# Optimization experiments

Measured on AMD Instinct MI355X. Metric: run time of the kernel, lower is better.

The kernel has to match this reference:

```python
import jax, jax.numpy as jnp
import numpy as np

HID = 1024
H = 8        # num_attention_heads
KV = 2       # num_key_value_heads
HD = HID // H  # head_dim = 128
G = H // KV    # kv groups = 4
EPS = 1e-6


def setup_inputs() -> dict:
    key = jax.random.key(0)
    ks = jax.random.split(key, 12)
    B, S = 4, 2048
    s = 0.02
    inp = {
        "hidden_states": jax.random.normal(ks[0], (B, S, HID), jnp.float32),
        "rope": jax.random.normal(ks[1], (1, 1, S, 2 * HD), jnp.float32),
        # q_proj outputs 2*H*HD (query + elementwise gate)
        "Wq": jax.random.normal(ks[2], (HID, 2 * H * HD), jnp.float32) * s,
        "bq": jnp.zeros((2 * H * HD,), jnp.float32),
        "Wk": jax.random.normal(ks[3], (HID, KV * HD), jnp.float32) * s,
        "bk": jnp.zeros((KV * HD,), jnp.float32),
        "Wv": jax.random.normal(ks[4], (HID, KV * HD), jnp.float32) * s,
        "bv": jnp.zeros((KV * HD,), jnp.float32),
        "Wo": jax.random.normal(ks[5], (H * HD, HID), jnp.float32) * s,
        "bo": jnp.zeros((HID,), jnp.float32),
        "q_norm_w": jnp.ones((HD,), jnp.float32),
        "k_norm_w": jnp.ones((HD,), jnp.float32),
    }
    return inp


def _rmsnorm(x, w):
    var = jnp.mean(jnp.square(x), axis=-1, keepdims=True)
    return x * jax.lax.rsqrt(var + EPS) * w


def _rot(x):
    # interleaved rotation: [-x1, x0, -x3, x2, ...]
    x2 = x.reshape(x.shape[:-1] + (HD // 2, 2))
    r = jnp.stack([-x2[..., 1], x2[..., 0]], axis=-1)
    return r.reshape(x.shape)


def _apply_rope_cat(x, emb):
    # emb: [S, 2*HD] = cat(sin, cos); x: [B, h, S, HD]
    sin, cos = jnp.split(emb, 2, axis=-1)
    sin = sin[None, None]
    cos = cos[None, None]
    return x * cos + _rot(x) * sin


def reference(hidden_states, rope, Wq, bq, Wk, bk, Wv, bv, Wo, bo, q_norm_w, k_norm_w):
    B, S, _ = hidden_states.shape
    qg = hidden_states @ Wq + bq                     # [B,S,2*H*HD]
    qg = qg.reshape(B, S, KV, -1)                    # [B,S,KV, 2*G*HD]
    q, gate = jnp.split(qg, [HD * G], axis=-1)       # [B,S,KV,G*HD], [B,S,KV,G*HD]
    gate = gate.reshape(B, S, H, HD)                 # [B,S,H,HD]
    q = q.reshape(B, S, H, HD).transpose(0, 2, 1, 3) # [B,H,S,HD]
    k = (hidden_states @ Wk + bk).reshape(B, S, KV, HD).transpose(0, 2, 1, 3)
    v = (hidden_states @ Wv + bv).reshape(B, S, KV, HD).transpose(0, 2, 1, 3)

    q = _rmsnorm(q, q_norm_w)
    k = _rmsnorm(k, k_norm_w)

    emb = rope[0, 0, :S]                             # [S, 2*HD]
    q = _apply_rope_cat(q, emb)
    k = _apply_rope_cat(k, emb)

    # GQA: repeat kv heads to match query heads
    k = jnp.repeat(k, G, axis=1)                     # [B,H,S,HD]
    v = jnp.repeat(v, G, axis=1)

    scale = 1.0 / jnp.sqrt(jnp.asarray(HD, q.dtype))
    scores = jnp.einsum("bhqd,bhkd->bhqk", q, k) * scale
    attn = jax.nn.softmax(scores, axis=-1)
    out = jnp.einsum("bhqk,bhkd->bhqd", attn, v)     # [B,H,S,HD]

    out = out.transpose(0, 2, 1, 3)                  # [B,S,H,HD]
    out = out * jax.nn.sigmoid(gate)
    out = out.reshape(B, S, H * HD)
    return out @ Wo + bo
```

## Files before the change

kernel.cpp:

```cpp
#include <hip/hip_runtime.h>
#include <math.h>

#define SCALE_ 0.08838834764831845f
#define PSHIFT 8.0f

typedef __attribute__((ext_vector_type(8))) short short8;
typedef __attribute__((ext_vector_type(4))) float floatx4;
typedef __attribute__((ext_vector_type(4))) _Float16 half4;
typedef __attribute__((ext_vector_type(8))) _Float16 half8;

__device__ inline short f2bf(float x) {
    union { float f; unsigned u; } v; v.f = x;
    unsigned r = v.u + 0x7fff + ((v.u >> 16) & 1);
    return (short)(r >> 16);
}
__device__ inline float bf2f(short h) {
    union { float f; unsigned u; } v; v.u = ((unsigned)(unsigned short)h) << 16;
    return v.f;
}

__global__ __launch_bounds__(256) void convert_x(
    const float* __restrict__ X, short* __restrict__ Xb,
    const float* __restrict__ bq, const float* __restrict__ bk2,
    const float* __restrict__ bv2, float* __restrict__ bcat)
{
    const int gid = blockIdx.x * 256 + threadIdx.x;
    if (gid < 2097152) {
        const float4 v = ((const float4*)X)[gid];
        short4 o;
        o.x = f2bf(v.x); o.y = f2bf(v.y); o.z = f2bf(v.z); o.w = f2bf(v.w);
        ((short4*)Xb)[gid] = o;
    }
    if (gid < 2560)
        bcat[gid] = (gid < 2048) ? bq[gid]
                  : (gid < 2304) ? bk2[gid - 2048] : bv2[gid - 2304];
}

__global__ __launch_bounds__(256) void wtrans(
    const float* __restrict__ Wq, const float* __restrict__ Wk,
    const float* __restrict__ Wv, const float* __restrict__ Wo,
    short* __restrict__ Wt, short* __restrict__ Wot)
{
    __shared__ float T[32][33];
    const int t = threadIdx.x;
    const int k0 = blockIdx.x * 32;
    const int ny = blockIdx.y;
    const float* src; int ldn, ncol0, nrow0; short* dst;
    if (ny < 80) {
        const int n0 = ny * 32;
        if (n0 < 2048)      { src = Wq; ldn = 2048; ncol0 = n0; }
        else if (n0 < 2304) { src = Wk; ldn = 256;  ncol0 = n0 - 2048; }
        else                { src = Wv; ldn = 256;  ncol0 = n0 - 2304; }
        dst = Wt; nrow0 = n0;
    } else {
        const int n0 = (ny - 80) * 32;
        src = Wo; ldn = 1024; ncol0 = n0; dst = Wot; nrow0 = n0;
    }
    {
        const int r = t >> 3, c4 = (t & 7) * 4;
        const float4 v = *(const float4*)&src[(size_t)(k0 + r) * ldn + ncol0 + c4];
        T[r][c4 + 0] = v.x; T[r][c4 + 1] = v.y; T[r][c4 + 2] = v.z; T[r][c4 + 3] = v.w;
    }
    __syncthreads();
    {
        const int nr = t >> 3, kc4 = (t & 7) * 4;
        short4 o;
        o.x = f2bf(T[kc4 + 0][nr]);
        o.y = f2bf(T[kc4 + 1][nr]);
        o.z = f2bf(T[kc4 + 2][nr]);
        o.w = f2bf(T[kc4 + 3][nr]);
        *(short4*)&dst[(size_t)(nrow0 + nr) * 1024 + k0 + kc4] = o;
    }
}

__global__ __launch_bounds__(256) void qkv_mfma(
    const short* __restrict__ Ag, const short* __restrict__ Bg,
    const float* __restrict__ bcat,
    short* __restrict__ qb, short* __restrict__ kb,
    short* __restrict__ vb, short* __restrict__ gateb)
{
    __shared__ short As[128 * 64];
    __shared__ short Bs[128 * 64];
    const int tid = threadIdx.x;
    const int wave = tid >> 6, lane = tid & 63;
    const int quad = lane >> 4, l16 = lane & 15;
    const int wm = wave & 1, wn = wave >> 1;
    const int m0 = blockIdx.y * 128, n0 = blockIdx.x * 128;

    floatx4 acc[4][4] = {};

    for (int k0 = 0; k0 < 1024; k0 += 64) {
        __syncthreads();
        #pragma unroll
        for (int c = 0; c < 4; ++c) {
            const int blk = (c * 4 + wave) * 64 + lane;
            const int row = blk >> 3, p = blk & 7;
            const int col = (p ^ (row & 7)) << 3;
            __builtin_amdgcn_global_load_lds(
                (const __attribute__((address_space(1))) unsigned int*)(Ag + (size_t)(m0 + row) * 1024 + k0 + col),
                (__attribute__((address_space(3))) unsigned int*)&As[(c * 4 + wave) * 512],
                16, 0, 0);
            __builtin_amdgcn_global_load_lds(
                (const __attribute__((address_space(1))) unsigned int*)(Bg + (size_t)(n0 + row) * 1024 + k0 + col),
                (__attribute__((address_space(3))) unsigned int*)&Bs[(c * 4 + wave) * 512],
                16, 0, 0);
        }
        __syncthreads();
        #pragma unroll
        for (int ks = 0; ks < 2; ++ks) {
            short8 af[4], bfr[4];
            #pragma unroll
            for (int mt = 0; mt < 4; ++mt) {
                const int row = wm * 64 + mt * 16 + l16;
                const int p = (ks * 4 + quad) ^ (row & 7);
                af[mt] = *(const short8*)&As[row * 64 + p * 8];
            }
            #pragma unroll
            for (int nt = 0; nt < 4; ++nt) {
                const int row = wn * 64 + nt * 16 + l16;
                const int p = (ks * 4 + quad) ^ (row & 7);
                bfr[nt] = *(const short8*)&Bs[row * 64 + p * 8];
            }
            #pragma unroll
            for (int mt = 0; mt < 4; ++mt)
                #pragma unroll
                for (int nt = 0; nt < 4; ++nt)
                    acc[mt][nt] = __builtin_amdgcn_mfma_f32_16x16x32_bf16(af[mt], bfr[nt], acc[mt][nt], 0, 0, 0);
        }
    }

    #pragma unroll
    for (int nt = 0; nt < 4; ++nt) {
        const int n = n0 + wn * 64 + nt * 16 + l16;
        const float bias = bcat[n];
        #pragma unroll
        for (int mt = 0; mt < 4; ++mt) {
            #pragma unroll
            for (int r = 0; r < 4; ++r) {
                const int m = m0 + wm * 64 + mt * 16 + quad * 4 + r;
                const int b = m >> 11, s = m & 2047;
                const short o = f2bf(acc[mt][nt][r] + bias);
                if (n < 2048) {
                    const int kv = n >> 10, rr = n & 1023;
                    if (rr < 512) {
                        const int h = kv * 4 + (rr >> 7), d = rr & 127;
                        qb[(((size_t)(b * 8 + h)) * 2048 + s) * 128 + d] = o;
                    } else {
                        const int r2 = rr - 512;
                        const int h = kv * 4 + (r2 >> 7), d = r2 & 127;
                        gateb[(size_t)m * 1024 + h * 128 + d] = o;
                    }
                } else if (n < 2304) {
                    const int c = n - 2048;
                    kb[(((size_t)(b * 2 + (c >> 7))) * 2048 + s) * 128 + (c & 127)] = o;
                } else {
                    const int c = n - 2304;
                    vb[(((size_t)(b * 2 + (c >> 7))) * 2048 + s) * 128 + (c & 127)] = o;
                }
            }
        }
    }
}

__global__ __launch_bounds__(256) void norm_rope(
    short* __restrict__ qb, short* __restrict__ kb,
    const float* __restrict__ rope,
    const float* __restrict__ qw, const float* __restrict__ kw)
{
    const int row = blockIdx.x * 4 + (threadIdx.x >> 6);
    short* base; const float* w; int s; float scl;
    if (row < 65536) { base = qb + (size_t)row * 128; s = row & 2047; w = qw; scl = SCALE_; }
    else { const int r2 = row - 65536; base = kb + (size_t)r2 * 128; s = r2 & 2047; w = kw; scl = 1.0f; }
    const int lane = threadIdx.x & 63;
    const short2 xv = *(const short2*)&base[lane * 2];
    const float x0 = bf2f(xv.x), x1 = bf2f(xv.y);
    float ssq = x0 * x0 + x1 * x1;
    #pragma unroll
    for (int off = 1; off < 64; off <<= 1) ssq += __shfl_xor(ssq, off);
    const float inv = rsqrtf(ssq * (1.0f / 128.0f) + 1e-6f);
    const float a = x0 * inv * w[lane * 2];
    const float b = x1 * inv * w[lane * 2 + 1];
    const float* er = rope + (size_t)s * 256;
    const float sin0 = er[lane * 2], sin1 = er[lane * 2 + 1];
    const float cos0 = er[128 + lane * 2], cos1 = er[128 + lane * 2 + 1];
    short2 o;
    o.x = f2bf((a * cos0 - b * sin0) * scl);
    o.y = f2bf((b * cos1 + a * sin1) * scl);
    *(short2*)&base[lane * 2] = o;
}

__global__ __launch_bounds__(256) void vtrans(
    const short* __restrict__ vb, _Float16* __restrict__ vt)
{
    __shared__ float T[32][33];
    const int t = threadIdx.x;
    const int s0 = blockIdx.x * 32, d0 = blockIdx.y * 32, bk = blockIdx.z;
    const short* src = vb + ((size_t)bk * 2048 + s0) * 128 + d0;
    {
        const int sr = t >> 3, c4 = (t & 7) * 4;
        const short4 xv = *(const short4*)&src[sr * 128 + c4];
        T[sr][c4 + 0] = bf2f(xv.x);
        T[sr][c4 + 1] = bf2f(xv.y);
        T[sr][c4 + 2] = bf2f(xv.z);
        T[sr][c4 + 3] = bf2f(xv.w);
    }
    __syncthreads();
    {
        const int dr = t >> 3, sc4 = (t & 7) * 4;
        const int cs = sc4 >> 2;
        const int nc = (cs < 4) ? (cs << 1) : (((cs - 4) << 1) | 1);
        half4 o;
        o[0] = (_Float16)T[sc4 + 0][dr];
        o[1] = (_Float16)T[sc4 + 1][dr];
        o[2] = (_Float16)T[sc4 + 2][dr];
        o[3] = (_Float16)T[sc4 + 3][dr];
        *(half4*)&vt[((size_t)bk * 128 + d0 + dr) * 2048 + s0 + nc * 4] = o;
    }
}

__global__ __launch_bounds__(256, 2) void attn_mfma(
    const short* __restrict__ qb, const short* __restrict__ kb,
    const _Float16* __restrict__ vt, const short* __restrict__ gateb,
    short* __restrict__ xo)
{
    __shared__ short    Ks[2][64 * 128];
    __shared__ _Float16 VTs[2][128 * 64];

    const int tid = threadIdx.x;
    const int wave = tid >> 6, lane = tid & 63;
    const int quad = lane >> 4, l16 = lane & 15;
    const int bh = blockIdx.y, b = bh >> 3, h = bh & 7, kv = h >> 2;
    const int q0 = blockIdx.x * 128;

    short8 qf[4][2];
    #pragma unroll
    for (int u = 0; u < 2; ++u) {
        const short* qbase = qb + (((size_t)(b * 8 + h)) * 2048 + q0 + wave * 32 + u * 16 + l16) * 128;
        #pragma unroll
        for (int ks = 0; ks < 4; ++ks)
            qf[ks][u] = *(const short8*)&qbase[ks * 32 + quad * 8];
    }

    const short*    kbase  = kb + (size_t)(b * 2 + kv) * 2048 * 128;
    const _Float16* vtbase = vt + (size_t)(b * 2 + kv) * 128 * 2048;

    int koff[4], voff[4];
    #pragma unroll
    for (int c = 0; c < 4; ++c) {
        const int idx = (c * 4 + wave) * 64 + lane;
        { const int r = idx >> 4, p = idx & 15;
          koff[c] = r * 128 + ((p ^ (r & 7)) << 3); }
        { const int r = idx >> 3, p = idx & 7;
          voff[c] = r * 2048 + ((p ^ (r & 7)) << 3); }
    }

    floatx4 O[8][2] = {};
    float lsum[2] = {0.0f, 0.0f};

    #pragma unroll
    for (int c = 0; c < 4; ++c) {
        __builtin_amdgcn_global_load_lds(
            (const __attribute__((address_space(1))) unsigned int*)(kbase + koff[c]),
            (__attribute__((address_space(3))) unsigned int*)&Ks[0][(c * 4 + wave) * 512],
            16, 0, 0);
        __builtin_amdgcn_global_load_lds(
            (const __attribute__((address_space(1))) unsigned int*)(vtbase + voff[c]),
            (__attribute__((address_space(3))) unsigned int*)&VTs[0][(c * 4 + wave) * 512],
            16, 0, 0);
    }

    for (int kt = 0; kt < 32; ++kt) {
        const int cur = kt & 1;
        __syncthreads();

        if (kt + 1 < 32) {
            const short*    kg = kbase  + (size_t)(kt + 1) * 8192;
            const _Float16* vg = vtbase + (kt + 1) * 64;
            #pragma unroll
            for (int c = 0; c < 4; ++c) {
                __builtin_amdgcn_global_load_lds(
                    (const __attribute__((address_space(1))) unsigned int*)(kg + koff[c]),
                    (__attribute__((address_space(3))) unsigned int*)&Ks[cur ^ 1][(c * 4 + wave) * 512],
                    16, 0, 0);
                __builtin_amdgcn_global_load_lds(
                    (const __attribute__((address_space(1))) unsigned int*)(vg + voff[c]),
                    (__attribute__((address_space(3))) unsigned int*)&VTs[cur ^ 1][(c * 4 + wave) * 512],
                    16, 0, 0);
            }
        }

        #pragma unroll
        for (int t = 0; t < 2; ++t) {
            floatx4 ST[2][2];
            #pragma unroll
            for (int j = 0; j < 2; ++j) {
                ST[j][0] = (floatx4){0.f, 0.f, 0.f, 0.f};
                ST[j][1] = (floatx4){0.f, 0.f, 0.f, 0.f};
                const int krow = (2 * t + j) * 16 + l16;
                #pragma unroll
                for (int ks = 0; ks < 4; ++ks) {
                    const short8 af = *(const short8*)&Ks[cur][krow * 128 + (((ks * 4 + quad) ^ (l16 & 7)) << 3)];
                    ST[j][0] = __builtin_amdgcn_mfma_f32_16x16x32_bf16(af, qf[ks][0], ST[j][0], 0, 0, 0);
                    ST[j][1] = __builtin_amdgcn_mfma_f32_16x16x32_bf16(af, qf[ks][1], ST[j][1], 0, 0, 0);
                }
            }

            half8 pf[2];
            #pragma unroll
            for (int u = 0; u < 2; ++u) {
                #pragma unroll
                for (int r = 0; r < 4; ++r) {
                    const float plo = __expf(ST[0][u][r] - PSHIFT);
                    const float phi = __expf(ST[1][u][r] - PSHIFT);
                    lsum[u] += plo + phi;
                    pf[u][r]     = (_Float16)plo;
                    pf[u][4 + r] = (_Float16)phi;
                }
            }

            #pragma unroll
            for (int dt = 0; dt < 8; ++dt) {
                const half8 va = *(const half8*)&VTs[cur][(dt * 16 + l16) * 64 + (((4 * t + quad) ^ (l16 & 7)) << 3)];
                O[dt][0] = __builtin_amdgcn_mfma_f32_16x16x32_f16(va, pf[0], O[dt][0], 0, 0, 0);
                O[dt][1] = __builtin_amdgcn_mfma_f32_16x16x32_f16(va, pf[1], O[dt][1], 0, 0, 0);
            }
        }
    }

    #pragma unroll
    for (int u = 0; u < 2; ++u) {
        float ps = lsum[u];
        ps += __shfl_xor(ps, 16);
        ps += __shfl_xor(ps, 32);
        const float invl = 1.0f / ps;
        const int s = q0 + wave * 32 + u * 16 + l16;
        const size_t base = ((size_t)b * 2048 + s) * 1024 + h * 128;
        #pragma unroll
        for (int dt = 0; dt < 8; ++dt) {
            const int d0 = dt * 16 + quad * 4;
            const short4 g4 = *(const short4*)&gateb[base + d0];
            short4 o4;
            o4.x = f2bf(O[dt][u][0] * invl * (1.0f / (1.0f + __expf(-bf2f(g4.x)))));
            o4.y = f2bf(O[dt][u][1] * invl * (1.0f / (1.0f + __expf(-bf2f(g4.y)))));
            o4.z = f2bf(O[dt][u][2] * invl * (1.0f / (1.0f + __expf(-bf2f(g4.z)))));
            o4.w = f2bf(O[dt][u][3] * invl * (1.0f / (1.0f + __expf(-bf2f(g4.w)))));
            *(short4*)&xo[base + d0] = o4;
        }
    }
}

__global__ __launch_bounds__(256) void out_mfma(
    const short* __restrict__ Ag, const short* __restrict__ Bg,
    const float* __restrict__ bo, float* __restrict__ Y)
{
    __shared__ short As[128 * 64];
    __shared__ short Bs[128 * 64];
    const int tid = threadIdx.x;
    const int wave = tid >> 6, lane = tid & 63;
    const int quad = lane >> 4, l16 = lane & 15;
    const int wm = wave & 1, wn = wave >> 1;
    const int m0 = blockIdx.y * 128, n0 = blockIdx.x * 128;

    floatx4 acc[4][4] = {};

    for (int k0 = 0; k0 < 1024; k0 += 64) {
        __syncthreads();
        #pragma unroll
        for (int c = 0; c < 4; ++c) {
            const int blk = (c * 4 + wave) * 64 + lane;
            const int row = blk >> 3, p = blk & 7;
            const int col = (p ^ (row & 7)) << 3;
            __builtin_amdgcn_global_load_lds(
                (const __attribute__((address_space(1))) unsigned int*)(Ag + (size_t)(m0 + row) * 1024 + k0 + col),
                (__attribute__((address_space(3))) unsigned int*)&As[(c * 4 + wave) * 512],
                16, 0, 0);
            __builtin_amdgcn_global_load_lds(
                (const __attribute__((address_space(1))) unsigned int*)(Bg + (size_t)(n0 + row) * 1024 + k0 + col),
                (__attribute__((address_space(3))) unsigned int*)&Bs[(c * 4 + wave) * 512],
                16, 0, 0);
        }
        __syncthreads();
        #pragma unroll
        for (int ks = 0; ks < 2; ++ks) {
            short8 af[4], bfr[4];
            #pragma unroll
            for (int mt = 0; mt < 4; ++mt) {
                const int row = wm * 64 + mt * 16 + l16;
                const int p = (ks * 4 + quad) ^ (row & 7);
                af[mt] = *(const short8*)&As[row * 64 + p * 8];
            }
            #pragma unroll
            for (int nt = 0; nt < 4; ++nt) {
                const int row = wn * 64 + nt * 16 + l16;
                const int p = (ks * 4 + quad) ^ (row & 7);
                bfr[nt] = *(const short8*)&Bs[row * 64 + p * 8];
            }
            #pragma unroll
            for (int mt = 0; mt < 4; ++mt)
                #pragma unroll
                for (int nt = 0; nt < 4; ++nt)
                    acc[mt][nt] = __builtin_amdgcn_mfma_f32_16x16x32_bf16(af[mt], bfr[nt], acc[mt][nt], 0, 0, 0);
        }
    }

    #pragma unroll
    for (int nt = 0; nt < 4; ++nt) {
        const int n = n0 + wn * 64 + nt * 16 + l16;
        const float bias = bo[n];
        #pragma unroll
        for (int mt = 0; mt < 4; ++mt) {
            #pragma unroll
            for (int r = 0; r < 4; ++r) {
                const int m = m0 + wm * 64 + mt * 16 + quad * 4 + r;
                Y[(size_t)m * 1024 + n] = acc[mt][nt][r] + bias;
            }
        }
    }
}

extern "C" void kernel_launch(void* const* d_in, const int* in_sizes, int n_in,
                              void* d_out, int out_size, void* d_ws, size_t ws_size,
                              hipStream_t stream) {
    (void)in_sizes; (void)n_in; (void)out_size; (void)ws_size;
    const float* hs   = (const float*)d_in[0];
    const float* rope = (const float*)d_in[1];
    const float* Wq   = (const float*)d_in[2];
    const float* bq   = (const float*)d_in[3];
    const float* Wk   = (const float*)d_in[4];
    const float* bk   = (const float*)d_in[5];
    const float* Wv   = (const float*)d_in[6];
    const float* bv   = (const float*)d_in[7];
    const float* Wo   = (const float*)d_in[8];
    const float* bo   = (const float*)d_in[9];
    const float* qw   = (const float*)d_in[10];
    const float* kw   = (const float*)d_in[11];
    float* out = (float*)d_out;

    short* qb    = (short*)d_ws;
    short* kbuf  = qb    + (size_t)8388608;
    short* vb    = kbuf  + (size_t)2097152;
    _Float16* vt = (_Float16*)(vb + (size_t)2097152);
    short* gateb = (short*)(vt + (size_t)2097152);
    short* xb    = gateb + (size_t)8388608;
    short* wt    = xb    + (size_t)8388608;
    short* wot   = wt    + (size_t)2621440;
    float* bcat  = (float*)(wot + (size_t)1048576);

    convert_x<<<dim3(8192), 256, 0, stream>>>(hs, xb, bq, bk, bv, bcat);
    wtrans<<<dim3(32, 112), 256, 0, stream>>>(Wq, Wk, Wv, Wo, wt, wot);
    qkv_mfma<<<dim3(20, 64), 256, 0, stream>>>(xb, wt, bcat, qb, kbuf, vb, gateb);
    norm_rope<<<dim3(20480), 256, 0, stream>>>(qb, kbuf, rope, qw, kw);
    vtrans<<<dim3(64, 4, 8), 256, 0, stream>>>(vb, vt);
    attn_mfma<<<dim3(16, 32), 256, 0, stream>>>(qb, kbuf, vt, gateb, xb);
    out_mfma<<<dim3(8, 64), 256, 0, stream>>>(xb, wot, bo, out);
}
```

Before: 298.3 us.

## Merge prep kernels, remap blocks for XCD locality, add MFMA priority and exp2 softmax

Combines convert_x with wtrans, and norm_rope with vtrans, so two launches are saved. The GEMM and attention grids are linearised and remapped so that blocks sharing A rows or a head land on the same XCD, which should improve L2 reuse. The attention inner loop raises wave priority around its MFMA sections and computes exp with exp2f of an FMA. These changes mix launch-overhead, locality and scheduling ideas, and the remaps depend on the eight-XCD round-robin dispatch assumption.

```diff
diff --git a/kernel.cpp b/kernel.cpp
--- a/kernel.cpp
+++ b/kernel.cpp
@@ -3,6 +3,8 @@
 
 #define SCALE_ 0.08838834764831845f
 #define PSHIFT 8.0f
+#define LOG2E_ 1.4426950408889634f
+#define PSH2_  11.541560327111707f
 
 typedef __attribute__((ext_vector_type(8))) short short8;
 typedef __attribute__((ext_vector_type(4))) float floatx4;
@@ -19,32 +21,33 @@
     return v.f;
 }
 
-__global__ __launch_bounds__(256) void convert_x(
+__global__ __launch_bounds__(256) void prep_fused(
     const float* __restrict__ X, short* __restrict__ Xb,
     const float* __restrict__ bq, const float* __restrict__ bk2,
-    const float* __restrict__ bv2, float* __restrict__ bcat)
-{
-    const int gid = blockIdx.x * 256 + threadIdx.x;
-    if (gid < 2097152) {
-        const float4 v = ((const float4*)X)[gid];
-        short4 o;
-        o.x = f2bf(v.x); o.y = f2bf(v.y); o.z = f2bf(v.z); o.w = f2bf(v.w);
-        ((short4*)Xb)[gid] = o;
-    }
-    if (gid < 2560)
-        bcat[gid] = (gid < 2048) ? bq[gid]
-                  : (gid < 2304) ? bk2[gid - 2048] : bv2[gid - 2304];
-}
-
-__global__ __launch_bounds__(256) void wtrans(
+    const float* __restrict__ bv2, float* __restrict__ bcat,
     const float* __restrict__ Wq, const float* __restrict__ Wk,
     const float* __restrict__ Wv, const float* __restrict__ Wo,
     short* __restrict__ Wt, short* __restrict__ Wot)
 {
     __shared__ float T[32][33];
+    const int bid = blockIdx.x;
     const int t = threadIdx.x;
-    const int k0 = blockIdx.x * 32;
-    const int ny = blockIdx.y;
+    if (bid < 8192) {
+        const int gid = bid * 256 + t;
+        if (gid < 2097152) {
+            const float4 v = ((const float4*)X)[gid];
+            short4 o;
+            o.x = f2bf(v.x); o.y = f2bf(v.y); o.z = f2bf(v.z); o.w = f2bf(v.w);
+            ((short4*)Xb)[gid] = o;
+        }
+        if (gid < 2560)
+            bcat[gid] = (gid < 2048) ? bq[gid]
+                      : (gid < 2304) ? bk2[gid - 2048] : bv2[gid - 2304];
+        return;
+    }
+    const int t2 = bid - 8192;
+    const int k0 = (t2 & 31) * 32;
+    const int ny = t2 >> 5;
     const float* src; int ldn, ncol0, nrow0; short* dst;
     if (ny < 80) {
         const int n0 = ny * 32;
@@ -85,7 +88,12 @@
     const int wave = tid >> 6, lane = tid & 63;
     const int quad = lane >> 4, l16 = lane & 15;
     const int wm = wave & 1, wn = wave >> 1;
-    const int m0 = blockIdx.y * 128, n0 = blockIdx.x * 128;
+    const int lin = blockIdx.x;
+    const int xcd = lin & 7;
+    const int idx = lin >> 3;
+    const int rr_ = idx / 20;
+    const int m0 = (xcd * 8 + rr_) * 128;
+    const int n0 = (idx - rr_ * 20) * 128;
 
     floatx4 acc[4][4] = {};
 
@@ -162,39 +170,40 @@
     }
 }
 
-__global__ __launch_bounds__(256) void norm_rope(
+__global__ __launch_bounds__(256) void norm_vtrans(
     short* __restrict__ qb, short* __restrict__ kb,
     const float* __restrict__ rope,
-    const float* __restrict__ qw, const float* __restrict__ kw)
-{
-    const int row = blockIdx.x * 4 + (threadIdx.x >> 6);
-    short* base; const float* w; int s; float scl;
-    if (row < 65536) { base = qb + (size_t)row * 128; s = row & 2047; w = qw; scl = SCALE_; }
-    else { const int r2 = row - 65536; base = kb + (size_t)r2 * 128; s = r2 & 2047; w = kw; scl = 1.0f; }
-    const int lane = threadIdx.x & 63;
-    const short2 xv = *(const short2*)&base[lane * 2];
-    const float x0 = bf2f(xv.x), x1 = bf2f(xv.y);
-    float ssq = x0 * x0 + x1 * x1;
-    #pragma unroll
-    for (int off = 1; off < 64; off <<= 1) ssq += __shfl_xor(ssq, off);
-    const float inv = rsqrtf(ssq * (1.0f / 128.0f) + 1e-6f);
-    const float a = x0 * inv * w[lane * 2];
-    const float b = x1 * inv * w[lane * 2 + 1];
-    const float* er = rope + (size_t)s * 256;
-    const float sin0 = er[lane * 2], sin1 = er[lane * 2 + 1];
-    const float cos0 = er[128 + lane * 2], cos1 = er[128 + lane * 2 + 1];
-    short2 o;
-    o.x = f2bf((a * cos0 - b * sin0) * scl);
-    o.y = f2bf((b * cos1 + a * sin1) * scl);
-    *(short2*)&base[lane * 2] = o;
-}
-
-__global__ __launch_bounds__(256) void vtrans(
+    const float* __restrict__ qw, const float* __restrict__ kw,
     const short* __restrict__ vb, _Float16* __restrict__ vt)
 {
     __shared__ float T[32][33];
+    const int bid = blockIdx.x;
     const int t = threadIdx.x;
-    const int s0 = blockIdx.x * 32, d0 = blockIdx.y * 32, bk = blockIdx.z;
+    if (bid < 20480) {
+        const int row = bid * 4 + (t >> 6);
+        short* base; const float* w; int s; float scl;
+        if (row < 65536) { base = qb + (size_t)row * 128; s = row & 2047; w = qw; scl = SCALE_; }
+        else { const int r2 = row - 65536; base = kb + (size_t)r2 * 128; s = r2 & 2047; w = kw; scl = 1.0f; }
+        const int lane = t & 63;
+        const short2 xv = *(const short2*)&base[lane * 2];
+        const float x0 = bf2f(xv.x), x1 = bf2f(xv.y);
+        float ssq = x0 * x0 + x1 * x1;
+        #pragma unroll
+        for (int off = 1; off < 64; off <<= 1) ssq += __shfl_xor(ssq, off);
+        const float inv = rsqrtf(ssq * (1.0f / 128.0f) + 1e-6f);
+        const float a = x0 * inv * w[lane * 2];
+        const float b = x1 * inv * w[lane * 2 + 1];
+        const float* er = rope + (size_t)s * 256;
+        const float sin0 = er[lane * 2], sin1 = er[lane * 2 + 1];
+        const float cos0 = er[128 + lane * 2], cos1 = er[128 + lane * 2 + 1];
+        short2 o;
+        o.x = f2bf((a * cos0 - b * sin0) * scl);
+        o.y = f2bf((b * cos1 + a * sin1) * scl);
+        *(short2*)&base[lane * 2] = o;
+        return;
+    }
+    const int t2 = bid - 20480;
+    const int s0 = (t2 & 63) * 32, d0 = ((t2 >> 6) & 3) * 32, bk = t2 >> 8;
     const short* src = vb + ((size_t)bk * 2048 + s0) * 128 + d0;
     {
         const int sr = t >> 3, c4 = (t & 7) * 4;
@@ -229,8 +238,11 @@
     const int tid = threadIdx.x;
     const int wave = tid >> 6, lane = tid & 63;
     const int quad = lane >> 4, l16 = lane & 15;
-    const int bh = blockIdx.y, b = bh >> 3, h = bh & 7, kv = h >> 2;
-    const int q0 = blockIdx.x * 128;
+    const int lin = blockIdx.x;
+    const int idx = lin >> 3;
+    const int bh = (lin & 7) * 4 + (idx >> 4);
+    const int b = bh >> 3, h = bh & 7, kv = h >> 2;
+    const int q0 = (idx & 15) * 128;
 
     short8 qf[4][2];
     #pragma unroll
@@ -247,10 +259,10 @@
     int koff[4], voff[4];
     #pragma unroll
     for (int c = 0; c < 4; ++c) {
-        const int idx = (c * 4 + wave) * 64 + lane;
-        { const int r = idx >> 4, p = idx & 15;
+        const int sidx = (c * 4 + wave) * 64 + lane;
+        { const int r = sidx >> 4, p = sidx & 15;
           koff[c] = r * 128 + ((p ^ (r & 7)) << 3); }
-        { const int r = idx >> 3, p = idx & 7;
+        { const int r = sidx >> 3, p = sidx & 7;
           voff[c] = r * 2048 + ((p ^ (r & 7)) << 3); }
     }
 
@@ -292,6 +304,7 @@
         #pragma unroll
         for (int t = 0; t < 2; ++t) {
             floatx4 ST[2][2];
+            __builtin_amdgcn_s_setprio(1);
             #pragma unroll
             for (int j = 0; j < 2; ++j) {
                 ST[j][0] = (floatx4){0.f, 0.f, 0.f, 0.f};
@@ -304,26 +317,29 @@
                     ST[j][1] = __builtin_amdgcn_mfma_f32_16x16x32_bf16(af, qf[ks][1], ST[j][1], 0, 0, 0);
                 }
             }
+            __builtin_amdgcn_s_setprio(0);
 
             half8 pf[2];
             #pragma unroll
             for (int u = 0; u < 2; ++u) {
                 #pragma unroll
                 for (int r = 0; r < 4; ++r) {
-                    const float plo = __expf(ST[0][u][r] - PSHIFT);
-                    const float phi = __expf(ST[1][u][r] - PSHIFT);
+                    const float plo = exp2f(fmaf(ST[0][u][r], LOG2E_, -PSH2_));
+                    const float phi = exp2f(fmaf(ST[1][u][r], LOG2E_, -PSH2_));
                     lsum[u] += plo + phi;
                     pf[u][r]     = (_Float16)plo;
                     pf[u][4 + r] = (_Float16)phi;
                 }
             }
 
+            __builtin_amdgcn_s_setprio(1);
             #pragma unroll
             for (int dt = 0; dt < 8; ++dt) {
                 const half8 va = *(const half8*)&VTs[cur][(dt * 16 + l16) * 64 + (((4 * t + quad) ^ (l16 & 7)) << 3)];
                 O[dt][0] = __builtin_amdgcn_mfma_f32_16x16x32_f16(va, pf[0], O[dt][0], 0, 0, 0);
                 O[dt][1] = __builtin_amdgcn_mfma_f32_16x16x32_f16(va, pf[1], O[dt][1], 0, 0, 0);
             }
+            __builtin_amdgcn_s_setprio(0);
         }
     }
 
@@ -359,7 +375,11 @@
     const int wave = tid >> 6, lane = tid & 63;
     const int quad = lane >> 4, l16 = lane & 15;
     const int wm = wave & 1, wn = wave >> 1;
-    const int m0 = blockIdx.y * 128, n0 = blockIdx.x * 128;
+    const int lin = blockIdx.x;
+    const int xcd = lin & 7;
+    const int idx = lin >> 3;
+    const int m0 = (xcd * 8 + (idx >> 3)) * 128;
+    const int n0 = (idx & 7) * 128;
 
     floatx4 acc[4][4] = {};
 
@@ -446,11 +466,10 @@
     short* wot   = wt    + (size_t)2621440;
     float* bcat  = (float*)(wot + (size_t)1048576);
 
-    convert_x<<<dim3(8192), 256, 0, stream>>>(hs, xb, bq, bk, bv, bcat);
-    wtrans<<<dim3(32, 112), 256, 0, stream>>>(Wq, Wk, Wv, Wo, wt, wot);
-    qkv_mfma<<<dim3(20, 64), 256, 0, stream>>>(xb, wt, bcat, qb, kbuf, vb, gateb);
-    norm_rope<<<dim3(20480), 256, 0, stream>>>(qb, kbuf, rope, qw, kw);
-    vtrans<<<dim3(64, 4, 8), 256, 0, stream>>>(vb, vt);
-    attn_mfma<<<dim3(16, 32), 256, 0, stream>>>(qb, kbuf, vt, gateb, xb);
-    out_mfma<<<dim3(8, 64), 256, 0, stream>>>(xb, wot, bo, out);
-}
+    prep_fused<<<dim3(11776), 256, 0, stream>>>(hs, xb, bq, bk, bv, bcat,
+                                                Wq, Wk, Wv, Wo, wt, wot);
+    qkv_mfma<<<dim3(1280), 256, 0, stream>>>(xb, wt, bcat, qb, kbuf, vb, gateb);
+    norm_vtrans<<<dim3(22528), 256, 0, stream>>>(qb, kbuf, rope, qw, kw, vb, vt);
+    attn_mfma<<<dim3(512), 256, 0, stream>>>(qb, kbuf, vt, gateb, xb);
+    out_mfma<<<dim3(512), 256, 0, stream>>>(xb, wot, bo, out);
+}
```

New measurement: 308.1 us. 3.3% more time.
